# Performance work log

Hardware: AMD Instinct MI355X
Metric: run time of the kernel (lower is better)

The kernel has to match this reference:

```python
import jax, jax.numpy as jnp
import numpy as np

IN_C, HID_C, OUT_C = 128, 256, 128
N_NODES, N_EDGES = 50000, 600000


def setup_inputs() -> dict:
    key = jax.random.key(0)
    ks = jax.random.split(key, 8)
    x = jax.random.normal(ks[0], (N_NODES, IN_C), dtype=jnp.float32)
    edge_index = jax.random.randint(ks[1], (2, N_EDGES), 0, N_NODES, dtype=jnp.int64)
    def glorot(k, shape):
        lim = np.sqrt(6.0 / (shape[0] + shape[1])).astype(np.float32)
        return jax.random.uniform(k, shape, dtype=jnp.float32, minval=-lim, maxval=lim)
    # PyG SAGEConv: out = lin_l(mean_aggr) + lin_r(x_root); bias only in lin_l
    W1_l = glorot(ks[2], (IN_C, HID_C)); b1 = jnp.zeros((HID_C,), jnp.float32)
    W1_r = glorot(ks[3], (IN_C, HID_C))
    W2_l = glorot(ks[4], (HID_C, OUT_C)); b2 = jnp.zeros((OUT_C,), jnp.float32)
    W2_r = glorot(ks[5], (HID_C, OUT_C))
    return {"x": x, "edge_index": edge_index, "W1_l": W1_l, "b1": b1, "W1_r": W1_r,
            "W2_l": W2_l, "b2": b2, "W2_r": W2_r}


def _sage_conv(x, src, dst, W_l, b, W_r):
    n = x.shape[0]
    msg = x[src]  # [E, C] gather from source nodes
    agg = jax.ops.segment_sum(msg, dst, num_segments=n)
    cnt = jax.ops.segment_sum(jnp.ones((src.shape[0],), x.dtype), dst, num_segments=n)
    agg = agg / jnp.maximum(cnt, 1.0)[:, None]  # mean aggregation, zero-deg safe
    return agg @ W_l + b + x @ W_r


def reference(x, edge_index, W1_l, b1, W1_r, W2_l, b2, W2_r):
    src, dst = edge_index[0], edge_index[1]
    h = jax.nn.relu(_sage_conv(x, src, dst, W1_l, b1, W1_r))
    return _sage_conv(h, src, dst, W2_l, b2, W2_r)
```

## Files before the change

### kernel.cpp

```cpp
#include <hip/hip_runtime.h>
#include <hip/hip_bf16.h>


#define N_NODES 50000
#define IN_C    128
#define HID_C   256
#define OUT_C   128
#define N_EDGES 600000

#define PB_CNT  2344
#define PB_W1   (PB_CNT + 256)
#define PB_W2   (PB_W1 + 256)
#define PB_X    (PB_W2 + 6250)

typedef __attribute__((ext_vector_type(8))) short short8;
typedef __attribute__((ext_vector_type(4))) float f32x4;
typedef __attribute__((ext_vector_type(2))) float f32x2;

__device__ __forceinline__ float bf2f(short s) {
    union { unsigned u; float f; } c;
    c.u = ((unsigned)(unsigned short)s) << 16;
    return c.f;
}
__device__ __forceinline__ unsigned f2fp8(float v) {
    return (unsigned)__builtin_amdgcn_cvt_pk_fp8_f32(v, v, 0, false) & 0xffu;
}
__device__ __forceinline__ void acc_fp8x4(float* a, unsigned u) {
    f32x2 lo = __builtin_amdgcn_cvt_pk_f32_fp8(u, false);
    f32x2 hi = __builtin_amdgcn_cvt_pk_f32_fp8(u, true);
    a[0] += lo[0]; a[1] += lo[1]; a[2] += hi[0]; a[3] += hi[1];
}

__global__ __launch_bounds__(256) void prep(
    const float* __restrict__ x, __hip_bfloat16* __restrict__ A1,
    const float* __restrict__ W1l, const float* __restrict__ W1r,
    const float* __restrict__ W2l, const float* __restrict__ W2r,
    __hip_bfloat16* __restrict__ W1t, __hip_bfloat16* __restrict__ W2t,
    const int* __restrict__ dstI, int* __restrict__ cnt) {
    int b = blockIdx.x;
    if (b < PB_CNT) {
        int e = b * 256 + threadIdx.x;
        if (e < N_EDGES) atomicAdd(&cnt[dstI[e]], 1);
    } else if (b < PB_W1) {
        int reg = b - PB_CNT;
        int half = reg >> 7;
        int t = (reg & 127) * 256 + threadIdx.x;
        int k = t >> 8, n = t & 255;
        const float* src = half ? W1r : W1l;
        W1t[n * 256 + half * 128 + k] = __float2bfloat16(src[t]);
    } else if (b < PB_W2) {
        int reg = b - PB_W1;
        int half = reg >> 7;
        int t = (reg & 127) * 256 + threadIdx.x;
        int k = t >> 7, n = t & 127;
        const float* src = half ? W2r : W2l;
        W2t[(size_t)(half * 128 + n) * 256 + k] = __float2bfloat16(src[t]);
    } else {
        int t = (b - PB_W2) * 256 + threadIdx.x;
        if (t >= N_NODES * 32) return;
        int row = t >> 5, c = (t & 31) * 4;
        float4 v = *(const float4*)(x + (size_t)row * 128 + c);
        __hip_bfloat16* d = A1 + (size_t)row * 256 + 128 + c;
        __hip_bfloat162 p0, p1;
        p0.x = __float2bfloat16(v.x); p0.y = __float2bfloat16(v.y);
        p1.x = __float2bfloat16(v.z); p1.y = __float2bfloat16(v.w);
        *(__hip_bfloat162*)d = p0;
        *(__hip_bfloat162*)(d + 2) = p1;
    }
}

__global__ __launch_bounds__(256) void assign_offsets(
    const int* __restrict__ cnt, int* __restrict__ row_ptr,
    int* __restrict__ cursor, int* __restrict__ total, int n) {
    __shared__ int tmp[256];
    __shared__ int sbase;
    int t = threadIdx.x, g = blockIdx.x * 256 + t;
    int v = (g < n) ? cnt[g] : 0;
    tmp[t] = v; __syncthreads();
    for (int off = 1; off < 256; off <<= 1) {
        int u = (t >= off) ? tmp[t - off] : 0;
        __syncthreads();
        tmp[t] += u;
        __syncthreads();
    }
    if (t == 255) sbase = atomicAdd(total, tmp[255]);
    __syncthreads();
    if (g < n) {
        int e = sbase + tmp[t] - v;
        row_ptr[g] = e;
        cursor[g] = e;
    }
}

__global__ void fill_csr(const int* __restrict__ srcI, const int* __restrict__ dstI,
                         int* __restrict__ cursor, int* __restrict__ col, int E) {
    int e = blockIdx.x * blockDim.x + threadIdx.x;
    if (e < E) {
        int pos = atomicAdd(&cursor[dstI[e]], 1);
        col[pos] = srcI[e];
    }
}

__global__ __launch_bounds__(256) void aggregate_bf16(
    const __hip_bfloat16* __restrict__ feat, int featStride,
    const int* __restrict__ row_ptr, const int* __restrict__ deg,
    const int* __restrict__ col,
    __hip_bfloat16* __restrict__ outp, int outStride, int nNodes) {
    int node = blockIdx.x * 16 + (threadIdx.x >> 4);
    int sl   = threadIdx.x & 15;
    if (node >= nNodes) return;
    int beg = row_ptr[node];
    int d   = deg[node];
    const __hip_bfloat16* base = feat + sl * 8;
    float a[8];
    #pragma unroll
    for (int c = 0; c < 8; ++c) a[c] = 0.f;

    short8 v0, v1, v2, v3;
    int j = 0;
    if (d >= 4) {
        int s0 = col[beg + 0], s1 = col[beg + 1];
        int s2 = col[beg + 2], s3 = col[beg + 3];
        v0 = *(const short8*)(base + (size_t)s0 * featStride);
        v1 = *(const short8*)(base + (size_t)s1 * featStride);
        v2 = *(const short8*)(base + (size_t)s2 * featStride);
        v3 = *(const short8*)(base + (size_t)s3 * featStride);
        for (; j + 8 <= d; j += 4) {
            int t0 = col[beg + j + 4], t1 = col[beg + j + 5];
            int t2 = col[beg + j + 6], t3 = col[beg + j + 7];
            short8 w0 = *(const short8*)(base + (size_t)t0 * featStride);
            short8 w1 = *(const short8*)(base + (size_t)t1 * featStride);
            short8 w2 = *(const short8*)(base + (size_t)t2 * featStride);
            short8 w3 = *(const short8*)(base + (size_t)t3 * featStride);
            #pragma unroll
            for (int c = 0; c < 8; ++c)
                a[c] += (bf2f(v0[c]) + bf2f(v1[c])) + (bf2f(v2[c]) + bf2f(v3[c]));
            v0 = w0; v1 = w1; v2 = w2; v3 = w3;
        }
        #pragma unroll
        for (int c = 0; c < 8; ++c)
            a[c] += (bf2f(v0[c]) + bf2f(v1[c])) + (bf2f(v2[c]) + bf2f(v3[c]));
        j += 4;
    }
    int rem = d - j;
    if (rem > 0) {
        int s0 = col[beg + j];
        int s1 = (rem > 1) ? col[beg + j + 1] : s0;
        int s2 = (rem > 2) ? col[beg + j + 2] : s0;
        short8 t0 = *(const short8*)(base + (size_t)s0 * featStride);
        short8 t1 = *(const short8*)(base + (size_t)s1 * featStride);
        short8 t2 = *(const short8*)(base + (size_t)s2 * featStride);
        #pragma unroll
        for (int c = 0; c < 8; ++c) a[c] += bf2f(t0[c]);
        if (rem > 1) {
            #pragma unroll
            for (int c = 0; c < 8; ++c) a[c] += bf2f(t1[c]);
        }
        if (rem > 2) {
            #pragma unroll
            for (int c = 0; c < 8; ++c) a[c] += bf2f(t2[c]);
        }
    }

    float inv = 1.f / (float)max(d, 1);
    __hip_bfloat16* o = outp + (size_t)node * outStride + sl * 8;
    short8 q;
    #pragma unroll
    for (int c = 0; c < 8; ++c) {
        union { __hip_bfloat16 b; short s; } cv;
        cv.b = __float2bfloat16(a[c] * inv);
        q[c] = cv.s;
    }
    *(short8*)o = q;
}

__global__ __launch_bounds__(256) void aggregate_fp8_final(
    const unsigned char* __restrict__ feat,
    const int* __restrict__ row_ptr, const int* __restrict__ deg,
    const int* __restrict__ col,
    float* __restrict__ outp, const float* __restrict__ pre, int nNodes) {
    int node = blockIdx.x * 16 + (threadIdx.x >> 4);
    int sl   = threadIdx.x & 15;
    if (node >= nNodes) return;
    int beg = row_ptr[node];
    int d   = deg[node];
    const unsigned char* base = feat + sl * 8;
    float a[8];
    #pragma unroll
    for (int c = 0; c < 8; ++c) a[c] = 0.f;

    uint2 v0, v1, v2, v3;
    int j = 0;
    if (d >= 4) {
        int s0 = col[beg + 0], s1 = col[beg + 1];
        int s2 = col[beg + 2], s3 = col[beg + 3];
        v0 = *(const uint2*)(base + (size_t)s0 * 128);
        v1 = *(const uint2*)(base + (size_t)s1 * 128);
        v2 = *(const uint2*)(base + (size_t)s2 * 128);
        v3 = *(const uint2*)(base + (size_t)s3 * 128);
        for (; j + 8 <= d; j += 4) {
            int t0 = col[beg + j + 4], t1 = col[beg + j + 5];
            int t2 = col[beg + j + 6], t3 = col[beg + j + 7];
            uint2 w0 = *(const uint2*)(base + (size_t)t0 * 128);
            uint2 w1 = *(const uint2*)(base + (size_t)t1 * 128);
            uint2 w2 = *(const uint2*)(base + (size_t)t2 * 128);
            uint2 w3 = *(const uint2*)(base + (size_t)t3 * 128);
            acc_fp8x4(a,     v0.x); acc_fp8x4(a,     v1.x);
            acc_fp8x4(a,     v2.x); acc_fp8x4(a,     v3.x);
            acc_fp8x4(a + 4, v0.y); acc_fp8x4(a + 4, v1.y);
            acc_fp8x4(a + 4, v2.y); acc_fp8x4(a + 4, v3.y);
            v0 = w0; v1 = w1; v2 = w2; v3 = w3;
        }
        acc_fp8x4(a,     v0.x); acc_fp8x4(a,     v1.x);
        acc_fp8x4(a,     v2.x); acc_fp8x4(a,     v3.x);
        acc_fp8x4(a + 4, v0.y); acc_fp8x4(a + 4, v1.y);
        acc_fp8x4(a + 4, v2.y); acc_fp8x4(a + 4, v3.y);
        j += 4;
    }
    for (; j < d; ++j) {
        uint2 v = *(const uint2*)(base + (size_t)col[beg + j] * 128);
        acc_fp8x4(a, v.x);
        acc_fp8x4(a + 4, v.y);
    }

    float inv = 1.f / (float)max(d, 1);
    const float* pp = pre + (size_t)node * 128 + sl * 8;
    float* op = outp + (size_t)node * 128 + sl * 8;
    float4 p0 = *(const float4*)pp;
    float4 p1 = *(const float4*)(pp + 4);
    *(float4*)op       = make_float4(a[0] * inv + p0.x, a[1] * inv + p0.y,
                                     a[2] * inv + p0.z, a[3] * inv + p0.w);
    *(float4*)(op + 4) = make_float4(a[4] * inv + p1.x, a[5] * inv + p1.y,
                                     a[6] * inv + p1.z, a[7] * inv + p1.w);
}


#define GBM 128
#define GBN 128
#define GBK 64
#define EP_STRIDE_BF 132

__device__ __forceinline__ void gload16(const void* g, void* l) {
    typedef const __attribute__((address_space(1))) unsigned int* gp_t;
    typedef __attribute__((address_space(3))) unsigned int* lp_t;
    __builtin_amdgcn_global_load_lds((gp_t)g, (lp_t)l, 16, 0, 0);
}

__global__ __launch_bounds__(256) void gemm_mfma(
    const __hip_bfloat16* __restrict__ A, int lda,
    const __hip_bfloat16* __restrict__ Bt,
    const float* __restrict__ bias,
    __hip_bfloat16* __restrict__ outBf,
    int M, int K) {
    __shared__ char sm[GBM * EP_STRIDE_BF * 2];
    __hip_bfloat16* Als = (__hip_bfloat16*)sm;
    __hip_bfloat16* Bls = (__hip_bfloat16*)(sm + GBM * GBK * 2);

    int tid  = threadIdx.x;
    int wave = tid >> 6, lane = tid & 63;
    int wm = wave >> 1, wn = wave & 1;
    int mb = blockIdx.x * GBM, nb = blockIdx.y * GBN;

    int srow_base = wave * 32;
    int lrow = lane >> 3;
    int pch  = lane & 7;

    f32x4 acc[4][4];
    #pragma unroll
    for (int i = 0; i < 4; ++i)
        #pragma unroll
        for (int j = 0; j < 4; ++j)
            acc[i][j] = (f32x4){0.f, 0.f, 0.f, 0.f};

    for (int kt = 0; kt < K; kt += GBK) {
        #pragma unroll
        for (int t = 0; t < 4; ++t) {
            int rloc = srow_base + t * 8 + lrow;
            int lch  = pch ^ (rloc & 7);
            int ga_row = mb + rloc; if (ga_row >= M) ga_row = M - 1;
            const __hip_bfloat16* ga = A + (size_t)ga_row * lda + kt + lch * 8;
            gload16(ga, &Als[(srow_base + t * 8) * GBK]);
            const __hip_bfloat16* gb = Bt + (size_t)(nb + rloc) * K + kt + lch * 8;
            gload16(gb, &Bls[(srow_base + t * 8) * GBK]);
        }
        __syncthreads();

        #pragma unroll
        for (int ks = 0; ks < GBK; ks += 32) {
            int chunkL = (ks >> 3) + (lane >> 4);
            short8 af[4], bf[4];
            #pragma unroll
            for (int i = 0; i < 4; ++i) {
                int row = wm * 64 + i * 16 + (lane & 15);
                int pc  = chunkL ^ (row & 7);
                af[i] = *(const short8*)&Als[row * GBK + pc * 8];
            }
            #pragma unroll
            for (int j = 0; j < 4; ++j) {
                int row = wn * 64 + j * 16 + (lane & 15);
                int pc  = chunkL ^ (row & 7);
                bf[j] = *(const short8*)&Bls[row * GBK + pc * 8];
            }
            #pragma unroll
            for (int i = 0; i < 4; ++i)
                #pragma unroll
                for (int j = 0; j < 4; ++j)
                    acc[i][j] = __builtin_amdgcn_mfma_f32_16x16x32_bf16(
                        af[i], bf[j], acc[i][j], 0, 0, 0);
        }
        __syncthreads();
    }

    int cn[4];
    float bc[4];
    __hip_bfloat16* sb = (__hip_bfloat16*)sm;
    #pragma unroll
    for (int j = 0; j < 4; ++j) {
        cn[j] = wn * 64 + j * 16 + (lane & 15);
        bc[j] = bias[nb + cn[j]];
    }
    #pragma unroll
    for (int i = 0; i < 4; ++i)
        #pragma unroll
        for (int r = 0; r < 4; ++r) {
            int lr = wm * 64 + i * 16 + (lane >> 4) * 4 + r;
            #pragma unroll
            for (int j = 0; j < 4; ++j)
                sb[lr * EP_STRIDE_BF + cn[j]] =
                    __float2bfloat16(fmaxf(acc[i][j][r] + bc[j], 0.f));
        }
    __syncthreads();
    #pragma unroll
    for (int it = 0; it < 8; ++it) {
        int chunk = it * 256 + tid;
        int lr  = chunk >> 4;
        int lcB = (chunk & 15) * 16;
        int grow = mb + lr;
        if (grow < M)
            *(float4*)((char*)outBf + (size_t)grow * 512 + nb * 2 + lcB) =
                *(const float4*)((const char*)sb + lr * (EP_STRIDE_BF * 2) + lcB);
    }
}

#define GBM2 64

__global__ __launch_bounds__(256) void gemm2_fused(
    const __hip_bfloat16* __restrict__ A,
    const __hip_bfloat16* __restrict__ Bt,
    const float* __restrict__ b2,
    unsigned char* __restrict__ outF8,
    float* __restrict__ outF,
    int M) {
    __shared__ __hip_bfloat16 Als[GBM2 * GBK];
    __shared__ __hip_bfloat16 Bls[256 * GBK];

    int tid  = threadIdx.x;
    int wave = tid >> 6, lane = tid & 63;
    int mb = blockIdx.x * GBM2;
    int lrow = lane >> 3;
    int pch  = lane & 7;

    f32x4 acc[4][4];
    #pragma unroll
    for (int i = 0; i < 4; ++i)
        #pragma unroll
        for (int j = 0; j < 4; ++j)
            acc[i][j] = (f32x4){0.f, 0.f, 0.f, 0.f};

    for (int kt = 0; kt < 256; kt += GBK) {
        #pragma unroll
        for (int t = 0; t < 2; ++t) {
            int g = wave * 2 + t;
            int rloc = g * 8 + lrow;
            int lch  = pch ^ (rloc & 7);
            int ga_row = mb + rloc; if (ga_row >= M) ga_row = M - 1;
            gload16(A + (size_t)ga_row * 256 + kt + lch * 8, &Als[g * 8 * GBK]);
        }
        #pragma unroll
        for (int t = 0; t < 8; ++t) {
            int g = wave * 8 + t;
            int rloc = g * 8 + lrow;
            int lch  = pch ^ (rloc & 7);
            gload16(Bt + (size_t)rloc * 256 + kt + lch * 8, &Bls[g * 8 * GBK]);
        }
        __syncthreads();

        #pragma unroll
        for (int ks = 0; ks < GBK; ks += 32) {
            int chunkL = (ks >> 3) + (lane >> 4);
            short8 af[4], bf[4];
            #pragma unroll
            for (int i = 0; i < 4; ++i) {
                int row = i * 16 + (lane & 15);
                int pc  = chunkL ^ (row & 7);
                af[i] = *(const short8*)&Als[row * GBK + pc * 8];
            }
            #pragma unroll
            for (int j = 0; j < 4; ++j) {
                int row = wave * 64 + j * 16 + (lane & 15);
                int pc  = chunkL ^ (row & 7);
                bf[j] = *(const short8*)&Bls[row * GBK + pc * 8];
            }
            #pragma unroll
            for (int i = 0; i < 4; ++i)
                #pragma unroll
                for (int j = 0; j < 4; ++j)
                    acc[i][j] = __builtin_amdgcn_mfma_f32_16x16x32_bf16(
                        af[i], bf[j], acc[i][j], 0, 0, 0);
        }
        __syncthreads();
    }

    int cn[4];
    #pragma unroll
    for (int j = 0; j < 4; ++j) cn[j] = wave * 64 + j * 16 + (lane & 15);
    if (wave < 2) {
        #pragma unroll
        for (int i = 0; i < 4; ++i)
            #pragma unroll
            for (int r = 0; r < 4; ++r) {
                int row = mb + i * 16 + (lane >> 4) * 4 + r;
                if (row >= M) continue;
                #pragma unroll
                for (int j = 0; j < 4; ++j)
                    outF8[(size_t)row * 128 + cn[j]] = (unsigned char)f2fp8(acc[i][j][r]);
            }
    } else {
        float bc[4];
        #pragma unroll
        for (int j = 0; j < 4; ++j) bc[j] = b2[cn[j] - 128];
        #pragma unroll
        for (int i = 0; i < 4; ++i)
            #pragma unroll
            for (int r = 0; r < 4; ++r) {
                int row = mb + i * 16 + (lane >> 4) * 4 + r;
                if (row >= M) continue;
                #pragma unroll
                for (int j = 0; j < 4; ++j)
                    outF[(size_t)row * 128 + cn[j] - 128] = acc[i][j][r] + bc[j];
            }
    }
}

extern "C" void kernel_launch(void* const* d_in, const int* in_sizes, int n_in,
                              void* d_out, int out_size, void* d_ws, size_t ws_size,
                              hipStream_t stream) {
    const float* x    = (const float*)d_in[0];
    const int*   ei   = (const int*)d_in[1];
    const float* W1l  = (const float*)d_in[2];
    const float* b1   = (const float*)d_in[3];
    const float* W1r  = (const float*)d_in[4];
    const float* W2l  = (const float*)d_in[5];
    const float* b2   = (const float*)d_in[6];
    const float* W2r  = (const float*)d_in[7];
    float* out = (float*)d_out;

    const int E = N_EDGES;
    const int N = N_NODES;
    const int* srcI = ei;
    const int* dstI = ei + E;

    char* w = (char*)d_ws;
    int*            cnt     = (int*)(w + 0);
    int*            total   = (int*)(w + 200000);
    int*            row_ptr = (int*)(w + 204800);
    int*            col     = (int*)(w + 409600);
    __hip_bfloat16* W1t     = (__hip_bfloat16*)(w + 2818048);
    __hip_bfloat16* W2t     = (__hip_bfloat16*)(w + 2949120);
    int*            cursor  = (int*)(w + 3080192);
    __hip_bfloat16* A1      = (__hip_bfloat16*)(w + 3280896);
    __hip_bfloat16* h_bf    = (__hip_bfloat16*)(w + 28880896);
    unsigned char*  hp_f8   = (unsigned char*)(w + 54480896);
    float*          pre     = (float*)(w + 67280896);

    hipMemsetAsync(cnt, 0, 200004, stream);
    prep<<<PB_X, 256, 0, stream>>>(x, A1, W1l, W1r, W2l, W2r, W1t, W2t, dstI, cnt);

    assign_offsets<<<(N + 255) / 256, 256, 0, stream>>>(cnt, row_ptr, cursor, total, N);
    fill_csr<<<(E + 255) / 256, 256, 0, stream>>>(srcI, dstI, cursor, col, E);

    aggregate_bf16<<<(N + 15) / 16, 256, 0, stream>>>(
        A1 + 128, 256, row_ptr, cnt, col, A1, 256, N);
    {
        dim3 grid((N + GBM - 1) / GBM, HID_C / GBN);
        gemm_mfma<<<grid, 256, 0, stream>>>(A1, 256, W1t, b1, h_bf, N, 256);
    }

    gemm2_fused<<<(N + GBM2 - 1) / GBM2, 256, 0, stream>>>(
        h_bf, W2t, b2, hp_f8, pre, N);

    aggregate_fp8_final<<<(N + 15) / 16, 256, 0, stream>>>(
        hp_f8, row_ptr, cnt, col, out, pre, N);
}
```

Measured before the change: 232.4 us.

## Partition gather feature tables into column slabs to improve cache locality

Stores the bf16 input features as four column partitions of 32 channels, and the fp8 layer-2 features as two partitions of 64 bytes. The aggregation kernels now run one grid slice per partition, so each gather pass touches a smaller table that fits better in L2/MALL. The first GEMM reads the root features from the partitioned layout and the aggregate from a separate 128-wide buffer. In exchange, each thread issues narrower 4-byte loads, and the CSR indices and row pointers are read once per partition.

Result: slower. 248.1 us (+6.8%).

```diff
diff --git a/kernel.cpp b/kernel.cpp
--- a/kernel.cpp
+++ b/kernel.cpp
@@ -17,10 +17,11 @@
 typedef __attribute__((ext_vector_type(4))) float f32x4;
 typedef __attribute__((ext_vector_type(2))) float f32x2;
 
-__device__ __forceinline__ float bf2f(short s) {
-    union { unsigned u; float f; } c;
-    c.u = ((unsigned)(unsigned short)s) << 16;
-    return c.f;
+__device__ __forceinline__ float bflo(unsigned u) {
+    union { unsigned x; float f; } c; c.x = u << 16; return c.f;
+}
+__device__ __forceinline__ float bfhi(unsigned u) {
+    union { unsigned x; float f; } c; c.x = u & 0xffff0000u; return c.f;
 }
 __device__ __forceinline__ unsigned f2fp8(float v) {
     return (unsigned)__builtin_amdgcn_cvt_pk_fp8_f32(v, v, 0, false) & 0xffu;
@@ -32,7 +33,7 @@
 }
 
 __global__ __launch_bounds__(256) void prep(
-    const float* __restrict__ x, __hip_bfloat16* __restrict__ A1,
+    const float* __restrict__ x, __hip_bfloat16* __restrict__ xq,
     const float* __restrict__ W1l, const float* __restrict__ W1r,
     const float* __restrict__ W2l, const float* __restrict__ W2r,
     __hip_bfloat16* __restrict__ W1t, __hip_bfloat16* __restrict__ W2t,
@@ -60,7 +61,8 @@
         if (t >= N_NODES * 32) return;
         int row = t >> 5, c = (t & 31) * 4;
         float4 v = *(const float4*)(x + (size_t)row * 128 + c);
-        __hip_bfloat16* d = A1 + (size_t)row * 256 + 128 + c;
+        __hip_bfloat16* d = xq + (size_t)(c >> 5) * (N_NODES * 32)
+                               + (size_t)row * 32 + (c & 31);
         __hip_bfloat162 p0, p1;
         p0.x = __float2bfloat16(v.x); p0.y = __float2bfloat16(v.y);
         p1.x = __float2bfloat16(v.z); p1.y = __float2bfloat16(v.w);
@@ -101,45 +103,42 @@
     }
 }
 
-__global__ __launch_bounds__(256) void aggregate_bf16(
-    const __hip_bfloat16* __restrict__ feat, int featStride,
+__global__ __launch_bounds__(256) void aggregate_l1(
+    const __hip_bfloat16* __restrict__ xq,
     const int* __restrict__ row_ptr, const int* __restrict__ deg,
     const int* __restrict__ col,
-    __hip_bfloat16* __restrict__ outp, int outStride, int nNodes) {
+    __hip_bfloat16* __restrict__ A1) {
+    int p = blockIdx.y;
     int node = blockIdx.x * 16 + (threadIdx.x >> 4);
     int sl   = threadIdx.x & 15;
-    if (node >= nNodes) return;
+    if (node >= N_NODES) return;
     int beg = row_ptr[node];
     int d   = deg[node];
-    const __hip_bfloat16* base = feat + sl * 8;
-    float a[8];
-    #pragma unroll
-    for (int c = 0; c < 8; ++c) a[c] = 0.f;
-
-    short8 v0, v1, v2, v3;
+    const __hip_bfloat16* tab = xq + (size_t)p * (N_NODES * 32) + sl * 2;
+    float a0 = 0.f, a1 = 0.f;
+
+    unsigned v0, v1, v2, v3;
     int j = 0;
     if (d >= 4) {
         int s0 = col[beg + 0], s1 = col[beg + 1];
         int s2 = col[beg + 2], s3 = col[beg + 3];
-        v0 = *(const short8*)(base + (size_t)s0 * featStride);
-        v1 = *(const short8*)(base + (size_t)s1 * featStride);
-        v2 = *(const short8*)(base + (size_t)s2 * featStride);
-        v3 = *(const short8*)(base + (size_t)s3 * featStride);
+        v0 = *(const unsigned*)(tab + (size_t)s0 * 32);
+        v1 = *(const unsigned*)(tab + (size_t)s1 * 32);
+        v2 = *(const unsigned*)(tab + (size_t)s2 * 32);
+        v3 = *(const unsigned*)(tab + (size_t)s3 * 32);
         for (; j + 8 <= d; j += 4) {
             int t0 = col[beg + j + 4], t1 = col[beg + j + 5];
             int t2 = col[beg + j + 6], t3 = col[beg + j + 7];
-            short8 w0 = *(const short8*)(base + (size_t)t0 * featStride);
-            short8 w1 = *(const short8*)(base + (size_t)t1 * featStride);
-            short8 w2 = *(const short8*)(base + (size_t)t2 * featStride);
-            short8 w3 = *(const short8*)(base + (size_t)t3 * featStride);
-            #pragma unroll
-            for (int c = 0; c < 8; ++c)
-                a[c] += (bf2f(v0[c]) + bf2f(v1[c])) + (bf2f(v2[c]) + bf2f(v3[c]));
+            unsigned w0 = *(const unsigned*)(tab + (size_t)t0 * 32);
+            unsigned w1 = *(const unsigned*)(tab + (size_t)t1 * 32);
+            unsigned w2 = *(const unsigned*)(tab + (size_t)t2 * 32);
+            unsigned w3 = *(const unsigned*)(tab + (size_t)t3 * 32);
+            a0 += (bflo(v0) + bflo(v1)) + (bflo(v2) + bflo(v3));
+            a1 += (bfhi(v0) + bfhi(v1)) + (bfhi(v2) + bfhi(v3));
             v0 = w0; v1 = w1; v2 = w2; v3 = w3;
         }
-        #pragma unroll
-        for (int c = 0; c < 8; ++c)
-            a[c] += (bf2f(v0[c]) + bf2f(v1[c])) + (bf2f(v2[c]) + bf2f(v3[c]));
+        a0 += (bflo(v0) + bflo(v1)) + (bflo(v2) + bflo(v3));
+        a1 += (bfhi(v0) + bfhi(v1)) + (bfhi(v2) + bfhi(v3));
         j += 4;
     }
     int rem = d - j;
@@ -147,91 +146,73 @@
         int s0 = col[beg + j];
         int s1 = (rem > 1) ? col[beg + j + 1] : s0;
         int s2 = (rem > 2) ? col[beg + j + 2] : s0;
-        short8 t0 = *(const short8*)(base + (size_t)s0 * featStride);
-        short8 t1 = *(const short8*)(base + (size_t)s1 * featStride);
-        short8 t2 = *(const short8*)(base + (size_t)s2 * featStride);
-        #pragma unroll
-        for (int c = 0; c < 8; ++c) a[c] += bf2f(t0[c]);
-        if (rem > 1) {
-            #pragma unroll
-            for (int c = 0; c < 8; ++c) a[c] += bf2f(t1[c]);
-        }
-        if (rem > 2) {
-            #pragma unroll
-            for (int c = 0; c < 8; ++c) a[c] += bf2f(t2[c]);
-        }
+        unsigned t0 = *(const unsigned*)(tab + (size_t)s0 * 32);
+        unsigned t1 = *(const unsigned*)(tab + (size_t)s1 * 32);
+        unsigned t2 = *(const unsigned*)(tab + (size_t)s2 * 32);
+        a0 += bflo(t0); a1 += bfhi(t0);
+        if (rem > 1) { a0 += bflo(t1); a1 += bfhi(t1); }
+        if (rem > 2) { a0 += bflo(t2); a1 += bfhi(t2); }
     }
 
     float inv = 1.f / (float)max(d, 1);
-    __hip_bfloat16* o = outp + (size_t)node * outStride + sl * 8;
-    short8 q;
-    #pragma unroll
-    for (int c = 0; c < 8; ++c) {
-        union { __hip_bfloat16 b; short s; } cv;
-        cv.b = __float2bfloat16(a[c] * inv);
-        q[c] = cv.s;
-    }
-    *(short8*)o = q;
-}
-
-__global__ __launch_bounds__(256) void aggregate_fp8_final(
-    const unsigned char* __restrict__ feat,
+    __hip_bfloat162 o;
+    o.x = __float2bfloat16(a0 * inv);
+    o.y = __float2bfloat16(a1 * inv);
+    *(__hip_bfloat162*)(A1 + (size_t)node * 128 + p * 32 + sl * 2) = o;
+}
+
+__global__ __launch_bounds__(256) void aggregate_final(
+    const unsigned char* __restrict__ hp2,
     const int* __restrict__ row_ptr, const int* __restrict__ deg,
     const int* __restrict__ col,
-    float* __restrict__ outp, const float* __restrict__ pre, int nNodes) {
+    const float* __restrict__ pre,
+    float* __restrict__ outp) {
+    int p = blockIdx.y;
     int node = blockIdx.x * 16 + (threadIdx.x >> 4);
     int sl   = threadIdx.x & 15;
-    if (node >= nNodes) return;
+    if (node >= N_NODES) return;
     int beg = row_ptr[node];
     int d   = deg[node];
-    const unsigned char* base = feat + sl * 8;
-    float a[8];
-    #pragma unroll
-    for (int c = 0; c < 8; ++c) a[c] = 0.f;
-
-    uint2 v0, v1, v2, v3;
+    const unsigned char* tab = hp2 + (size_t)p * (N_NODES * 64) + sl * 4;
+    float a[4];
+    #pragma unroll
+    for (int c = 0; c < 4; ++c) a[c] = 0.f;
+
+    unsigned v0, v1, v2, v3;
     int j = 0;
     if (d >= 4) {
         int s0 = col[beg + 0], s1 = col[beg + 1];
         int s2 = col[beg + 2], s3 = col[beg + 3];
-        v0 = *(const uint2*)(base + (size_t)s0 * 128);
-        v1 = *(const uint2*)(base + (size_t)s1 * 128);
-        v2 = *(const uint2*)(base + (size_t)s2 * 128);
-        v3 = *(const uint2*)(base + (size_t)s3 * 128);
+        v0 = *(const unsigned*)(tab + (size_t)s0 * 64);
+        v1 = *(const unsigned*)(tab + (size_t)s1 * 64);
+        v2 = *(const unsigned*)(tab + (size_t)s2 * 64);
+        v3 = *(const unsigned*)(tab + (size_t)s3 * 64);
         for (; j + 8 <= d; j += 4) {
             int t0 = col[beg + j + 4], t1 = col[beg + j + 5];
             int t2 = col[beg + j + 6], t3 = col[beg + j + 7];
-            uint2 w0 = *(const uint2*)(base + (size_t)t0 * 128);
-            uint2 w1 = *(const uint2*)(base + (size_t)t1 * 128);
-            uint2 w2 = *(const uint2*)(base + (size_t)t2 * 128);
-            uint2 w3 = *(const uint2*)(base + (size_t)t3 * 128);
-            acc_fp8x4(a,     v0.x); acc_fp8x4(a,     v1.x);
-            acc_fp8x4(a,     v2.x); acc_fp8x4(a,     v3.x);
-            acc_fp8x4(a + 4, v0.y); acc_fp8x4(a + 4, v1.y);
-            acc_fp8x4(a + 4, v2.y); acc_fp8x4(a + 4, v3.y);
+            unsigned w0 = *(const unsigned*)(tab + (size_t)t0 * 64);
+            unsigned w1 = *(const unsigned*)(tab + (size_t)t1 * 64);
+            unsigned w2 = *(const unsigned*)(tab + (size_t)t2 * 64);
+            unsigned w3 = *(const unsigned*)(tab + (size_t)t3 * 64);
+            acc_fp8x4(a, v0); acc_fp8x4(a, v1);
+            acc_fp8x4(a, v2); acc_fp8x4(a, v3);
             v0 = w0; v1 = w1; v2 = w2; v3 = w3;
         }
-        acc_fp8x4(a,     v0.x); acc_fp8x4(a,     v1.x);
-        acc_fp8x4(a,     v2.x); acc_fp8x4(a,     v3.x);
-        acc_fp8x4(a + 4, v0.y); acc_fp8x4(a + 4, v1.y);
-        acc_fp8x4(a + 4, v2.y); acc_fp8x4(a + 4, v3.y);
+        acc_fp8x4(a, v0); acc_fp8x4(a, v1);
+        acc_fp8x4(a, v2); acc_fp8x4(a, v3);
         j += 4;
     }
     for (; j < d; ++j) {
-        uint2 v = *(const uint2*)(base + (size_t)col[beg + j] * 128);
-        acc_fp8x4(a, v.x);
-        acc_fp8x4(a + 4, v.y);
+        unsigned v = *(const unsigned*)(tab + (size_t)col[beg + j] * 64);
+        acc_fp8x4(a, v);
     }
 
     float inv = 1.f / (float)max(d, 1);
-    const float* pp = pre + (size_t)node * 128 + sl * 8;
-    float* op = outp + (size_t)node * 128 + sl * 8;
+    const float* pp = pre + (size_t)node * 128 + p * 64 + sl * 4;
     float4 p0 = *(const float4*)pp;
-    float4 p1 = *(const float4*)(pp + 4);
-    *(float4*)op       = make_float4(a[0] * inv + p0.x, a[1] * inv + p0.y,
-                                     a[2] * inv + p0.z, a[3] * inv + p0.w);
-    *(float4*)(op + 4) = make_float4(a[4] * inv + p1.x, a[5] * inv + p1.y,
-                                     a[6] * inv + p1.z, a[7] * inv + p1.w);
+    *(float4*)(outp + (size_t)node * 128 + p * 64 + sl * 4) =
+        make_float4(a[0] * inv + p0.x, a[1] * inv + p0.y,
+                    a[2] * inv + p0.z, a[3] * inv + p0.w);
 }
 
 
@@ -247,11 +228,12 @@
 }
 
 __global__ __launch_bounds__(256) void gemm_mfma(
-    const __hip_bfloat16* __restrict__ A, int lda,
+    const __hip_bfloat16* __restrict__ A1,
+    const __hip_bfloat16* __restrict__ xq,
     const __hip_bfloat16* __restrict__ Bt,
     const float* __restrict__ bias,
     __hip_bfloat16* __restrict__ outBf,
-    int M, int K) {
+    int M) {
     __shared__ char sm[GBM * EP_STRIDE_BF * 2];
     __hip_bfloat16* Als = (__hip_bfloat16*)sm;
     __hip_bfloat16* Bls = (__hip_bfloat16*)(sm + GBM * GBK * 2);
@@ -272,15 +254,22 @@
         for (int j = 0; j < 4; ++j)
             acc[i][j] = (f32x4){0.f, 0.f, 0.f, 0.f};
 
-    for (int kt = 0; kt < K; kt += GBK) {
+    for (int kt = 0; kt < 256; kt += GBK) {
         #pragma unroll
         for (int t = 0; t < 4; ++t) {
             int rloc = srow_base + t * 8 + lrow;
             int lch  = pch ^ (rloc & 7);
             int ga_row = mb + rloc; if (ga_row >= M) ga_row = M - 1;
-            const __hip_bfloat16* ga = A + (size_t)ga_row * lda + kt + lch * 8;
+            const __hip_bfloat16* ga;
+            if (kt < 128) {
+                ga = A1 + (size_t)ga_row * 128 + kt + lch * 8;
+            } else {
+                int chunk = ((kt - 128) >> 5) + (lch >> 2);
+                ga = xq + (size_t)chunk * (N_NODES * 32)
+                        + (size_t)ga_row * 32 + (lch & 3) * 8;
+            }
             gload16(ga, &Als[(srow_base + t * 8) * GBK]);
-            const __hip_bfloat16* gb = Bt + (size_t)(nb + rloc) * K + kt + lch * 8;
+            const __hip_bfloat16* gb = Bt + (size_t)(nb + rloc) * 256 + kt + lch * 8;
             gload16(gb, &Bls[(srow_base + t * 8) * GBK]);
         }
         __syncthreads();
@@ -349,7 +338,7 @@
     const __hip_bfloat16* __restrict__ Bt,
     const float* __restrict__ b2,
     unsigned char* __restrict__ outF8,
-    float* __restrict__ outF,
+    float* __restrict__ pre,
     int M) {
     __shared__ __hip_bfloat16 Als[GBM2 * GBK];
     __shared__ __hip_bfloat16 Bls[256 * GBK];
@@ -411,10 +400,8 @@
         __syncthreads();
     }
 
-    int cn[4];
-    #pragma unroll
-    for (int j = 0; j < 4; ++j) cn[j] = wave * 64 + j * 16 + (lane & 15);
     if (wave < 2) {
+        unsigned char* hb = outF8 + (size_t)wave * (N_NODES * 64);
         #pragma unroll
         for (int i = 0; i < 4; ++i)
             #pragma unroll
@@ -423,12 +410,14 @@
                 if (row >= M) continue;
                 #pragma unroll
                 for (int j = 0; j < 4; ++j)
-                    outF8[(size_t)row * 128 + cn[j]] = (unsigned char)f2fp8(acc[i][j][r]);
+                    hb[(size_t)row * 64 + j * 16 + (lane & 15)] =
+                        (unsigned char)f2fp8(acc[i][j][r]);
             }
     } else {
+        int cbase = (wave - 2) * 64;
         float bc[4];
         #pragma unroll
-        for (int j = 0; j < 4; ++j) bc[j] = b2[cn[j] - 128];
+        for (int j = 0; j < 4; ++j) bc[j] = b2[cbase + j * 16 + (lane & 15)];
         #pragma unroll
         for (int i = 0; i < 4; ++i)
             #pragma unroll
@@ -437,7 +426,8 @@
                 if (row >= M) continue;
                 #pragma unroll
                 for (int j = 0; j < 4; ++j)
-                    outF[(size_t)row * 128 + cn[j] - 128] = acc[i][j][r] + bc[j];
+                    pre[(size_t)row * 128 + cbase + j * 16 + (lane & 15)] =
+                        acc[i][j][r] + bc[j];
             }
     }
 }
@@ -469,26 +459,27 @@
     __hip_bfloat16* W2t     = (__hip_bfloat16*)(w + 2949120);
     int*            cursor  = (int*)(w + 3080192);
     __hip_bfloat16* A1      = (__hip_bfloat16*)(w + 3280896);
+    __hip_bfloat16* xq      = (__hip_bfloat16*)(w + 16080896);
     __hip_bfloat16* h_bf    = (__hip_bfloat16*)(w + 28880896);
-    unsigned char*  hp_f8   = (unsigned char*)(w + 54480896);
-    float*          pre     = (float*)(w + 67280896);
+    unsigned char*  hp2     = (unsigned char*)(w + 54480896);
+    float*          pre     = (float*)(w + 60880896);
 
     hipMemsetAsync(cnt, 0, 200004, stream);
-    prep<<<PB_X, 256, 0, stream>>>(x, A1, W1l, W1r, W2l, W2r, W1t, W2t, dstI, cnt);
+    prep<<<PB_X, 256, 0, stream>>>(x, xq, W1l, W1r, W2l, W2r, W1t, W2t, dstI, cnt);
 
     assign_offsets<<<(N + 255) / 256, 256, 0, stream>>>(cnt, row_ptr, cursor, total, N);
     fill_csr<<<(E + 255) / 256, 256, 0, stream>>>(srcI, dstI, cursor, col, E);
 
-    aggregate_bf16<<<(N + 15) / 16, 256, 0, stream>>>(
-        A1 + 128, 256, row_ptr, cnt, col, A1, 256, N);
+    aggregate_l1<<<dim3((N + 15) / 16, 4), 256, 0, stream>>>(
+        xq, row_ptr, cnt, col, A1);
     {
         dim3 grid((N + GBM - 1) / GBM, HID_C / GBN);
-        gemm_mfma<<<grid, 256, 0, stream>>>(A1, 256, W1t, b1, h_bf, N, 256);
+        gemm_mfma<<<grid, 256, 0, stream>>>(A1, xq, W1t, b1, h_bf, N);
     }
 
     gemm2_fused<<<(N + GBM2 - 1) / GBM2, 256, 0, stream>>>(
-        h_bf, W2t, b2, hp_f8, pre, N);
-
-    aggregate_fp8_final<<<(N + 15) / 16, 256, 0, stream>>>(
-        hp_f8, row_ptr, cnt, col, out, pre, N);
-}
+        h_bf, W2t, b2, hp2, pre, N);
+
+    aggregate_final<<<dim3((N + 15) / 16, 2), 256, 0, stream>>>(
+        hp2, row_ptr, cnt, col, pre, out);
+}
```

## Schedule aggregation nodes in descending-degree order via bucketed permutation

Applied to the files above, without the earlier changes.

Builds a per-degree histogram during offset assignment, scans it in a small single-block kernel, and scatters node ids into a permutation sorted by descending degree (capped at 63), striped over 16 sub-buckets. Both aggregation kernels then process nodes through this permutation, so the 16-lane groups in a block handle nodes of similar degree. This is meant to reduce load imbalance and lane divergence within blocks. The cost is an extra kernel launch, histogram atomics, an indirection load per node, and scattered output writes.

Result: slower. 415.2 us (+78.7%).

```diff
diff --git a/kernel.cpp b/kernel.cpp
--- a/kernel.cpp
+++ b/kernel.cpp
@@ -12,6 +12,9 @@
 #define PB_W1   (PB_CNT + 256)
 #define PB_W2   (PB_W1 + 256)
 #define PB_X    (PB_W2 + 6250)
+
+#define FB_EDGE 2344
+#define FB_PERM (FB_EDGE + 196)
 
 typedef __attribute__((ext_vector_type(8))) short short8;
 typedef __attribute__((ext_vector_type(4))) float f32x4;
@@ -71,11 +74,16 @@
 
 __global__ __launch_bounds__(256) void assign_offsets(
     const int* __restrict__ cnt, int* __restrict__ row_ptr,
-    int* __restrict__ cursor, int* __restrict__ total, int n) {
+    int* __restrict__ cursor, int* __restrict__ total,
+    int* __restrict__ hist, int n) {
     __shared__ int tmp[256];
     __shared__ int sbase;
     int t = threadIdx.x, g = blockIdx.x * 256 + t;
     int v = (g < n) ? cnt[g] : 0;
+    if (g < n) {
+        int bk = 63 - (v < 63 ? v : 63);
+        atomicAdd(&hist[bk * 16 + (blockIdx.x & 15)], 1);
+    }
     tmp[t] = v; __syncthreads();
     for (int off = 1; off < 256; off <<= 1) {
         int u = (t >= off) ? tmp[t - off] : 0;
@@ -92,23 +100,58 @@
     }
 }
 
-__global__ void fill_csr(const int* __restrict__ srcI, const int* __restrict__ dstI,
-                         int* __restrict__ cursor, int* __restrict__ col, int E) {
-    int e = blockIdx.x * blockDim.x + threadIdx.x;
-    if (e < E) {
-        int pos = atomicAdd(&cursor[dstI[e]], 1);
-        col[pos] = srcI[e];
+__global__ __launch_bounds__(64) void bucket_scan(
+    const int* __restrict__ hist, int* __restrict__ bcur) {
+    __shared__ int tot[64];
+    int b = threadIdx.x;
+    int loc[16];
+    int s = 0;
+    #pragma unroll
+    for (int k = 0; k < 16; ++k) { loc[k] = s; s += hist[b * 16 + k]; }
+    tot[b] = s; __syncthreads();
+    for (int off = 1; off < 64; off <<= 1) {
+        int u = (b >= off) ? tot[b - off] : 0;
+        __syncthreads();
+        tot[b] += u;
+        __syncthreads();
+    }
+    int base = tot[b] - s;
+    #pragma unroll
+    for (int k = 0; k < 16; ++k) bcur[b * 16 + k] = base + loc[k];
+}
+
+__global__ __launch_bounds__(256) void fill_csr_perm(
+    const int* __restrict__ srcI, const int* __restrict__ dstI,
+    int* __restrict__ cursor, int* __restrict__ col,
+    const int* __restrict__ cnt, int* __restrict__ bcur,
+    int* __restrict__ perm) {
+    int b = blockIdx.x;
+    if (b < FB_EDGE) {
+        int e = b * 256 + threadIdx.x;
+        if (e < N_EDGES) {
+            int pos = atomicAdd(&cursor[dstI[e]], 1);
+            col[pos] = srcI[e];
+        }
+    } else {
+        int i = (b - FB_EDGE) * 256 + threadIdx.x;
+        if (i < N_NODES) {
+            int d = cnt[i];
+            int bk = 63 - (d < 63 ? d : 63);
+            int pos = atomicAdd(&bcur[bk * 16 + ((i >> 8) & 15)], 1);
+            perm[pos] = i;
+        }
     }
 }
 
 __global__ __launch_bounds__(256) void aggregate_bf16(
     const __hip_bfloat16* __restrict__ feat, int featStride,
     const int* __restrict__ row_ptr, const int* __restrict__ deg,
-    const int* __restrict__ col,
+    const int* __restrict__ col, const int* __restrict__ perm,
     __hip_bfloat16* __restrict__ outp, int outStride, int nNodes) {
-    int node = blockIdx.x * 16 + (threadIdx.x >> 4);
+    int slot = blockIdx.x * 16 + (threadIdx.x >> 4);
     int sl   = threadIdx.x & 15;
-    if (node >= nNodes) return;
+    if (slot >= nNodes) return;
+    int node = perm[slot];
     int beg = row_ptr[node];
     int d   = deg[node];
     const __hip_bfloat16* base = feat + sl * 8;
@@ -177,11 +220,12 @@
 __global__ __launch_bounds__(256) void aggregate_fp8_final(
     const unsigned char* __restrict__ feat,
     const int* __restrict__ row_ptr, const int* __restrict__ deg,
-    const int* __restrict__ col,
+    const int* __restrict__ col, const int* __restrict__ perm,
     float* __restrict__ outp, const float* __restrict__ pre, int nNodes) {
-    int node = blockIdx.x * 16 + (threadIdx.x >> 4);
+    int slot = blockIdx.x * 16 + (threadIdx.x >> 4);
     int sl   = threadIdx.x & 15;
-    if (node >= nNodes) return;
+    if (slot >= nNodes) return;
+    int node = perm[slot];
     int beg = row_ptr[node];
     int d   = deg[node];
     const unsigned char* base = feat + sl * 8;
@@ -463,24 +507,30 @@
     char* w = (char*)d_ws;
     int*            cnt     = (int*)(w + 0);
     int*            total   = (int*)(w + 200000);
+    int*            hist    = (int*)(w + 200704);
     int*            row_ptr = (int*)(w + 204800);
     int*            col     = (int*)(w + 409600);
     __hip_bfloat16* W1t     = (__hip_bfloat16*)(w + 2818048);
     __hip_bfloat16* W2t     = (__hip_bfloat16*)(w + 2949120);
     int*            cursor  = (int*)(w + 3080192);
-    __hip_bfloat16* A1      = (__hip_bfloat16*)(w + 3280896);
-    __hip_bfloat16* h_bf    = (__hip_bfloat16*)(w + 28880896);
-    unsigned char*  hp_f8   = (unsigned char*)(w + 54480896);
-    float*          pre     = (float*)(w + 67280896);
-
-    hipMemsetAsync(cnt, 0, 200004, stream);
+    int*            bcur    = (int*)(w + 3280192);
+    int*            perm    = (int*)(w + 3284288);
+    __hip_bfloat16* A1      = (__hip_bfloat16*)(w + 3484288);
+    __hip_bfloat16* h_bf    = (__hip_bfloat16*)(w + 29084288);
+    unsigned char*  hp_f8   = (unsigned char*)(w + 54684288);
+    float*          pre     = (float*)(w + 61084288);
+
+    hipMemsetAsync(cnt, 0, 204800, stream);
     prep<<<PB_X, 256, 0, stream>>>(x, A1, W1l, W1r, W2l, W2r, W1t, W2t, dstI, cnt);
 
-    assign_offsets<<<(N + 255) / 256, 256, 0, stream>>>(cnt, row_ptr, cursor, total, N);
-    fill_csr<<<(E + 255) / 256, 256, 0, stream>>>(srcI, dstI, cursor, col, E);
+    assign_offsets<<<(N + 255) / 256, 256, 0, stream>>>(
+        cnt, row_ptr, cursor, total, hist, N);
+    bucket_scan<<<1, 64, 0, stream>>>(hist, bcur);
+    fill_csr_perm<<<FB_PERM, 256, 0, stream>>>(
+        srcI, dstI, cursor, col, cnt, bcur, perm);
 
     aggregate_bf16<<<(N + 15) / 16, 256, 0, stream>>>(
-        A1 + 128, 256, row_ptr, cnt, col, A1, 256, N);
+        A1 + 128, 256, row_ptr, cnt, col, perm, A1, 256, N);
     {
         dim3 grid((N + GBM - 1) / GBM, HID_C / GBN);
         gemm_mfma<<<grid, 256, 0, stream>>>(A1, 256, W1t, b1, h_bf, N, 256);
@@ -490,5 +540,5 @@
         h_bf, W2t, b2, hp_f8, pre, N);
 
     aggregate_fp8_final<<<(N + 15) / 16, 256, 0, stream>>>(
-        hp_f8, row_ptr, cnt, col, out, pre, N);
-}
+        hp_f8, row_ptr, cnt, col, perm, out, pre, N);
+}
```
